# Kernel tuning notes

Measured on AMD Instinct MI355X. Metric: run time of the kernel, lower is better.

The kernel has to match this reference:

```python
import jax, jax.numpy as jnp
import numpy as np

EPS = 1e-5

def _layernorm(x, g, b):
    mu = jnp.mean(x, axis=-1, keepdims=True)
    var = jnp.mean((x - mu) ** 2, axis=-1, keepdims=True)
    return (x - mu) / jnp.sqrt(var + EPS) * g + b


def setup_inputs() -> dict:
    key = jax.random.key(0)
    ks = jax.random.split(key, 4)
    B, H, W, C = 8, 96, 96, 256
    return {
        "x1": jax.random.normal(ks[0], (B, H, W, C), dtype=jnp.float32),
        "x2": jax.random.normal(ks[1], (B, H, W, C), dtype=jnp.float32),
        # norm1 (shared LayerNorm applied to both x1 and x2)
        "g1": jnp.ones((C,), jnp.float32),
        "b1": jnp.zeros((C,), jnp.float32),
        # reprojection 1x1 conv: C -> 2C
        "Wr": jax.random.normal(ks[2], (2 * C, C), dtype=jnp.float32) * 0.05,
        "br": jnp.zeros((2 * C,), jnp.float32),
        # final LayerNorm over 2C
        "g2": jnp.ones((2 * C,), jnp.float32),
        "b2": jnp.zeros((2 * C,), jnp.float32),
        # learnable mixing scalars
        "a1": jnp.array(0.25, jnp.float32),
        "a2": jnp.array(0.25, jnp.float32),
        "a3": jnp.array(0.25, jnp.float32),
        "a4": jnp.array(0.25, jnpp_ := jnp.float32),
    }


def reference(x1, x2, g1, b1, Wr, br, g2, b2, a1, a2, a3, a4):
    B, H, W, C = x1.shape
    N, D = H * W, C  # head_count = 1, key_channels = value_channels = D
    n1 = _layernorm(x1.reshape(B, N, C), g1, b1)  # [B,N,D]
    n2 = _layernorm(x2.reshape(B, N, C), g1, b1)

    kq = jnp.swapaxes(n2, 1, 2)                   # [B,D,N]
    key_sm = jax.nn.softmax(kq, axis=2)           # softmax over N
    query = jax.nn.softmax(kq, axis=1)            # softmax over D
    value = jnp.swapaxes(n1, 1, 2)                # [B,D,N]

    # context = key @ value^T : [B,D,D]
    context = jnp.einsum('bdn,ben->bde', key_sm, value)

    def masked_softmax(k):
        # torch.topk + scatter mask == keep entries >= k-th largest per row
        thr = jax.lax.top_k(context, k)[0][..., -1:]
        return jax.nn.softmax(jnp.where(context >= thr, context, -jnp.inf), axis=-1)

    ks = [D // 2, (D * 2) // 3, (D * 3) // 4, (D * 4) // 5]
    o = [jnp.einsum('bde,ben->bdn', masked_softmax(k), query) for k in ks]
    att = a1 * o[0] + a2 * o[1] + a3 * o[2] + a4 * o[3]  # [B,D,N]

    # 1x1 conv reprojection D -> 2D, then LayerNorm over channels
    rep = jnp.einsum('oc,bcn->bno', Wr, att) + br         # [B,N,2D]
    rep = _layernorm(rep, g2, b2)
    # view(B,H,W,2C).permute(0,3,1,2)
    return jnp.transpose(rep.reshape(B, H, W, 2 * C), (0, 3, 1, 2))
```

## Files before the change

### kernel.cpp

```cpp
#include <hip/hip_runtime.h>
#include <hip/hip_bf16.h>

#define Bc 8
#define Nn 9216
#define Dd 256
#define Oo 512
#define EPSc 1e-5f

#define OFF_MU1    0
#define OFF_RSTD1  73728
#define OFF_MU2    147456
#define OFF_RSTD2  221184
#define OFF_ROWINV 294912
#define OFF_COLSUM 368640
#define OFF_M      894976
#define OFF_W2T    1419264
#define OFF_CTXP   2467840

typedef __attribute__((ext_vector_type(4))) float f32x4;
typedef __attribute__((ext_vector_type(8))) short short8;
typedef __attribute__((ext_vector_type(8))) unsigned short ushort8;

static __device__ __forceinline__ unsigned short f2bf(float f) {
    __hip_bfloat16 h = __float2bfloat16(f);
    union { __hip_bfloat16 hh; unsigned short uu; } cv; cv.hh = h;
    return cv.uu;
}

#define SWZ(ch) (((((ch) >> 2) & 7)) ^ ((((ch) & 3)) << 1))

__global__ __launch_bounds__(256) void mg_k0_zero(float* __restrict__ p, int n4) {
    int i = blockIdx.x * 256 + threadIdx.x;
    if (i < n4) ((float4*)p)[i] = make_float4(0.f, 0.f, 0.f, 0.f);
}

__global__ __launch_bounds__(256) void mg_k1_stats(const float* __restrict__ x1, const float* __restrict__ x2,
                                                   const float* __restrict__ g1, const float* __restrict__ b1,
                                                   float* __restrict__ ws)
{
    float* mu1    = ws + OFF_MU1;
    float* rstd1  = ws + OFF_RSTD1;
    float* mu2    = ws + OFF_MU2;
    float* rstd2  = ws + OFF_RSTD2;
    float* rowinv = ws + OFF_ROWINV;
    float* colsum = ws + OFF_COLSUM;

    int t = threadIdx.x, lane = t & 63, w = t >> 6;
    int b = blockIdx.x / 144, rb = blockIdx.x % 144;
    int nbase = rb * 64;

    float4 g1v = ((const float4*)g1)[lane];
    float4 b1v = ((const float4*)b1)[lane];
    float cs0 = 0.f, cs1 = 0.f, cs2 = 0.f, cs3 = 0.f;
    __shared__ float csL[4][256];

    for (int i = 0; i < 16; ++i) {
        int n = nbase + i * 4 + w;
        int base = (b * Nn + n) * 64 + lane;
        float4 xa = ((const float4*)x1)[base];
        float4 xb = ((const float4*)x2)[base];
        float s1 = xa.x + xa.y + xa.z + xa.w;
        float q1 = xa.x*xa.x + xa.y*xa.y + xa.z*xa.z + xa.w*xa.w;
        float s2 = xb.x + xb.y + xb.z + xb.w;
        float q2 = xb.x*xb.x + xb.y*xb.y + xb.z*xb.z + xb.w*xb.w;
        #pragma unroll
        for (int m = 1; m < 64; m <<= 1) {
            s1 += __shfl_xor(s1, m); q1 += __shfl_xor(q1, m);
            s2 += __shfl_xor(s2, m); q2 += __shfl_xor(q2, m);
        }
        float m1 = s1 * (1.f / Dd), m2 = s2 * (1.f / Dd);
        float r1 = rsqrtf(q1 * (1.f / Dd) - m1 * m1 + EPSc);
        float r2 = rsqrtf(q2 * (1.f / Dd) - m2 * m2 + EPSc);
        int ni = b * Nn + n;
        if (lane == 0) { mu1[ni] = m1; rstd1[ni] = r1; mu2[ni] = m2; rstd2[ni] = r2; }
        float e0 = __expf((xb.x - m2) * r2 * g1v.x + b1v.x);
        float e1 = __expf((xb.y - m2) * r2 * g1v.y + b1v.y);
        float e2 = __expf((xb.z - m2) * r2 * g1v.z + b1v.z);
        float e3 = __expf((xb.w - m2) * r2 * g1v.w + b1v.w);
        float rs = e0 + e1 + e2 + e3;
        #pragma unroll
        for (int m = 1; m < 64; m <<= 1) rs += __shfl_xor(rs, m);
        if (lane == 0) rowinv[ni] = 1.f / rs;
        cs0 += e0; cs1 += e1; cs2 += e2; cs3 += e3;
    }
    csL[w][lane * 4 + 0] = cs0;
    csL[w][lane * 4 + 1] = cs1;
    csL[w][lane * 4 + 2] = cs2;
    csL[w][lane * 4 + 3] = cs3;
    __syncthreads();
    float tot = csL[0][t] + csL[1][t] + csL[2][t] + csL[3][t];
    atomicAdd(&colsum[b * Dd + t], tot);
}

__global__ __launch_bounds__(512, 2) void mg_k3_ctx(const float* __restrict__ x1, const float* __restrict__ x2,
                                                    const float* __restrict__ g1, const float* __restrict__ b1,
                                                    float* __restrict__ ws, int nks)
{
    __shared__ ushort PA[256 * 64];
    __shared__ ushort PB[256 * 64];
    const float* mu1   = ws + OFF_MU1;
    const float* rstd1 = ws + OFF_RSTD1;
    const float* mu2   = ws + OFF_MU2;
    const float* rstd2 = ws + OFF_RSTD2;
    float* ctxp = ws + OFF_CTXP;

    int t = threadIdx.x;
    int ks_i = blockIdx.x % nks;
    int b = blockIdx.x / nks;
    int krange = Nn / nks;
    int ntiles = krange >> 6;
    int n_base = ks_i * krange;

    int o  = t >> 6;
    int c4 = t & 63;

    f32x4 g1v = ((const f32x4*)g1)[c4];
    f32x4 b1v = ((const f32x4*)b1)[c4];

    int lane = t & 63, wave = t >> 6;
    int wd = wave & 3, we = wave >> 2;
    int l15 = lane & 15, kgrp = lane >> 4;

    f32x4 acc[4][8];
    #pragma unroll
    for (int dt = 0; dt < 4; ++dt)
        #pragma unroll
        for (int et = 0; et < 8; ++et) acc[dt][et] = (f32x4){0.f, 0.f, 0.f, 0.f};

    for (int st = 0; st < ntiles; ++st) {
        int rowb = b * Nn + n_base + st * 64 + o * 8;
        __syncthreads();
        {
            f32x4 mv0 = *(const f32x4*)(mu1 + rowb),   mv1 = *(const f32x4*)(mu1 + rowb + 4);
            f32x4 rv0 = *(const f32x4*)(rstd1 + rowb), rv1 = *(const f32x4*)(rstd1 + rowb + 4);
            float mva[8] = {mv0[0], mv0[1], mv0[2], mv0[3], mv1[0], mv1[1], mv1[2], mv1[3]};
            float rva[8] = {rv0[0], rv0[1], rv0[2], rv0[3], rv1[0], rv1[1], rv1[2], rv1[3]};
            f32x4 xv[8];
            #pragma unroll
            for (int rr = 0; rr < 8; ++rr)
                xv[rr] = ((const f32x4*)x1)[(size_t)(rowb + rr) * 64 + c4];
            #pragma unroll
            for (int i = 0; i < 4; ++i) {
                int ch = c4 * 4 + i;
                ushort8 u;
                #pragma unroll
                for (int rr = 0; rr < 8; ++rr)
                    u[rr] = f2bf((xv[rr][i] - mva[rr]) * rva[rr] * g1v[i] + b1v[i]);
                *(ushort8*)&PB[ch * 64 + ((o + SWZ(ch)) & 7) * 8] = u;
            }
        }
        {
            f32x4 mv0 = *(const f32x4*)(mu2 + rowb),   mv1 = *(const f32x4*)(mu2 + rowb + 4);
            f32x4 rv0 = *(const f32x4*)(rstd2 + rowb), rv1 = *(const f32x4*)(rstd2 + rowb + 4);
            float mva[8] = {mv0[0], mv0[1], mv0[2], mv0[3], mv1[0], mv1[1], mv1[2], mv1[3]};
            float rva[8] = {rv0[0], rv0[1], rv0[2], rv0[3], rv1[0], rv1[1], rv1[2], rv1[3]};
            f32x4 xv[8];
            #pragma unroll
            for (int rr = 0; rr < 8; ++rr)
                xv[rr] = ((const f32x4*)x2)[(size_t)(rowb + rr) * 64 + c4];
            #pragma unroll
            for (int i = 0; i < 4; ++i) {
                int ch = c4 * 4 + i;
                ushort8 u;
                #pragma unroll
                for (int rr = 0; rr < 8; ++rr)
                    u[rr] = f2bf(__expf((xv[rr][i] - mva[rr]) * rva[rr] * g1v[i] + b1v[i]));
                *(ushort8*)&PA[ch * 64 + ((o + SWZ(ch)) & 7) * 8] = u;
            }
        }
        __syncthreads();

        #pragma unroll
        for (int kk = 0; kk < 2; ++kk) {
            short8 af[4], bf[8];
            #pragma unroll
            for (int dt = 0; dt < 4; ++dt) {
                int ch = wd * 64 + dt * 16 + l15;
                af[dt] = *(const short8*)&PA[ch * 64 + (((kk << 2) + kgrp + SWZ(ch)) & 7) * 8];
            }
            #pragma unroll
            for (int et = 0; et < 8; ++et) {
                int ch = we * 128 + et * 16 + l15;
                bf[et] = *(const short8*)&PB[ch * 64 + (((kk << 2) + kgrp + SWZ(ch)) & 7) * 8];
            }
            #pragma unroll
            for (int dt = 0; dt < 4; ++dt)
                #pragma unroll
                for (int et = 0; et < 8; ++et)
                    acc[dt][et] = __builtin_amdgcn_mfma_f32_16x16x32_bf16(af[dt], bf[et], acc[dt][et], 0, 0, 0);
        }
    }

    size_t obase = ((size_t)ks_i * Bc + b) * (Dd * Dd);
    #pragma unroll
    for (int dt = 0; dt < 4; ++dt) {
        #pragma unroll
        for (int r = 0; r < 4; ++r) {
            int d = wd * 64 + dt * 16 + kgrp * 4 + r;
            float* rowp = ctxp + obase + (size_t)d * Dd + we * 128 + l15;
            #pragma unroll
            for (int et = 0; et < 8; ++et)
                rowp[et * 16] = acc[dt][et][r];
        }
    }
}

__global__ __launch_bounds__(256) void mg_k5_mask(const float* __restrict__ a1p, const float* __restrict__ a2p,
                                                  const float* __restrict__ a3p, const float* __restrict__ a4p,
                                                  float* __restrict__ ws, int nks)
{
    const float* ctxp   = ws + OFF_CTXP;
    const float* colsum = ws + OFF_COLSUM;
    float* Mo = ws + OFF_M;
    int t = threadIdx.x;
    int b = blockIdx.x >> 8, d = blockIdx.x & 255;
    __shared__ float s[256];
    __shared__ float wred[4][4];

    float c = 0.f;
    for (int p = 0; p < nks; ++p)
        c += ctxp[((size_t)p * Bc + b) * (Dd * Dd) + (size_t)d * Dd + t];
    float inv = 1.f / colsum[b * Dd + d];
    c *= inv;
    s[t] = c;
    __syncthreads();
    for (int k = 2; k <= 256; k <<= 1) {
        for (int j = k >> 1; j > 0; j >>= 1) {
            int ixj = t ^ j;
            if (ixj > t) {
                float A = s[t], Bv = s[ixj];
                bool desc = ((t & k) == 0);
                bool sw = desc ? (A < Bv) : (A > Bv);
                if (sw) { s[t] = Bv; s[ixj] = A; }
            }
            __syncthreads();
        }
    }
    float cmax = s[0];
    float t0 = s[127], t1 = s[169], t2 = s[191], t3 = s[203];
    float e = __expf(c - cmax);
    float w0 = (c >= t0) ? e : 0.f;
    float w1 = (c >= t1) ? e : 0.f;
    float w2 = (c >= t2) ? e : 0.f;
    float w3 = (c >= t3) ? e : 0.f;
    float v0 = w0, v1 = w1, v2 = w2, v3 = w3;
    #pragma unroll
    for (int m = 1; m < 64; m <<= 1) {
        v0 += __shfl_xor(v0, m); v1 += __shfl_xor(v1, m);
        v2 += __shfl_xor(v2, m); v3 += __shfl_xor(v3, m);
    }
    int lane = t & 63, wv = t >> 6;
    if (lane == 0) { wred[wv][0] = v0; wred[wv][1] = v1; wred[wv][2] = v2; wred[wv][3] = v3; }
    __syncthreads();
    float S0 = wred[0][0] + wred[1][0] + wred[2][0] + wred[3][0];
    float S1 = wred[0][1] + wred[1][1] + wred[2][1] + wred[3][1];
    float S2 = wred[0][2] + wred[1][2] + wred[2][2] + wred[3][2];
    float S3 = wred[0][3] + wred[1][3] + wred[2][3] + wred[3][3];
    float Mv = a1p[0] * (w0 / S0) + a2p[0] * (w1 / S1) + a3p[0] * (w2 / S2) + a4p[0] * (w3 / S3);
    Mo[(b * Dd + d) * Dd + t] = Mv;
}

__global__ __launch_bounds__(256) void mg_k6_w2(const float* __restrict__ Wr, float* __restrict__ ws)
{
    const float* Mo = ws + OFF_M;
    ushort* W2B = (ushort*)(ws + OFF_W2T);
    __shared__ float Mt[32][128];
    __shared__ float WrT[32][36];
    int t = threadIdx.x;
    int b = blockIdx.x >> 5, ob = (blockIdx.x >> 1) & 15, eh = blockIdx.x & 1;
    int o0 = ob * 32, e0 = eh * 128;
    int ol4 = t & 7, el = t >> 3;
    float acc[4][4];
    #pragma unroll
    for (int i = 0; i < 4; ++i)
        #pragma unroll
        for (int j = 0; j < 4; ++j) acc[i][j] = 0.f;

    for (int ch = 0; ch < 8; ++ch) {
        int c0 = ch * 32;
        __syncthreads();
        #pragma unroll
        for (int k = 0; k < 4; ++k) {
            int fi = t + k * 256;
            int row = fi >> 5, c4 = fi & 31;
            float4 mv = ((const float4*)Mo)[(b * Dd + c0 + row) * 64 + (e0 >> 2) + c4];
            *(float4*)&Mt[row][c4 * 4] = mv;
        }
        {
            int ol = t >> 3, c4 = t & 7;
            float4 wv = ((const float4*)Wr)[(o0 + ol) * 64 + (c0 >> 2) + c4];
            WrT[c4 * 4 + 0][ol] = wv.x;
            WrT[c4 * 4 + 1][ol] = wv.y;
            WrT[c4 * 4 + 2][ol] = wv.z;
            WrT[c4 * 4 + 3][ol] = wv.w;
        }
        __syncthreads();
        #pragma unroll
        for (int cc = 0; cc < 32; ++cc) {
            float4 w4 = *(const float4*)&WrT[cc][ol4 * 4];
            float4 m4 = *(const float4*)&Mt[cc][el * 4];
            float wv[4] = {w4.x, w4.y, w4.z, w4.w};
            float mv[4] = {m4.x, m4.y, m4.z, m4.w};
            #pragma unroll
            for (int i = 0; i < 4; ++i)
                #pragma unroll
                for (int j = 0; j < 4; ++j)
                    acc[i][j] = fmaf(wv[i], mv[j], acc[i][j]);
        }
    }
    #pragma unroll
    for (int i = 0; i < 4; ++i) {
        int o = o0 + ol4 * 4 + i;
        ushort4 u;
        u.x = f2bf(acc[i][0]); u.y = f2bf(acc[i][1]);
        u.z = f2bf(acc[i][2]); u.w = f2bf(acc[i][3]);
        *(ushort4*)&W2B[((size_t)b * Oo + o) * Dd + e0 + el * 4] = u;
    }
}

__global__ __launch_bounds__(256, 2) void mg_k7_final(const float* __restrict__ x2,
        const float* __restrict__ g1, const float* __restrict__ b1,
        const float* __restrict__ br, const float* __restrict__ g2, const float* __restrict__ b2,
        const float* __restrict__ ws, float* __restrict__ out)
{
    __shared__ ushort qsT[64 * 256];
    __shared__ float stat[4][4][16][2];
    __shared__ float musig[64][2];

    const float* mu2    = ws + OFF_MU2;
    const float* rstd2  = ws + OFF_RSTD2;
    const float* rowinv = ws + OFF_ROWINV;
    const ushort* W2B   = (const ushort*)(ws + OFF_W2T);

    int t = threadIdx.x;
    int b = blockIdx.x / 144, nt0 = blockIdx.x % 144;
    int n0 = nt0 * 64;

    {
        int row = t >> 2, gb = (t & 3) * 8;
        int ni = b * Nn + n0 + row;
        float m = mu2[ni], r = rstd2[ni], ri = rowinv[ni];
        #pragma unroll
        for (int j = 0; j < 8; ++j) {
            int g = gb + j;
            int e = g * 8;
            const float4* xp = (const float4*)x2 + (size_t)ni * 64 + g * 2;
            float4 xa = xp[0], xb = xp[1];
            float4 ga = ((const float4*)g1)[g * 2], gb4 = ((const float4*)g1)[g * 2 + 1];
            float4 ba = ((const float4*)b1)[g * 2], bb4 = ((const float4*)b1)[g * 2 + 1];
            float v[8]  = {xa.x, xa.y, xa.z, xa.w, xb.x, xb.y, xb.z, xb.w};
            float gv[8] = {ga.x, ga.y, ga.z, ga.w, gb4.x, gb4.y, gb4.z, gb4.w};
            float bv[8] = {ba.x, ba.y, ba.z, ba.w, bb4.x, bb4.y, bb4.z, bb4.w};
            ushort8 u;
            #pragma unroll
            for (int q = 0; q < 8; ++q)
                u[q] = f2bf(__expf((v[q] - m) * r * gv[q] + bv[q]) * ri);
            (void)e;
            *(ushort8*)&qsT[row * 256 + ((g ^ (row & 7)) << 3)] = u;
        }
    }
    __syncthreads();

    int lw = t & 63, wave = t >> 6;
    int colA = lw & 15, kgrp = lw >> 4;

    f32x4 acc[8][4];
    #pragma unroll
    for (int ot = 0; ot < 8; ++ot)
        #pragma unroll
        for (int nt = 0; nt < 4; ++nt)
            acc[ot][nt] = (f32x4){0.f, 0.f, 0.f, 0.f};

    const ushort* abase = W2B + ((size_t)b * Oo + wave * 128 + colA) * Dd + kgrp * 8;

#define LOADAF(dst, ksv)                                                        \
    {                                                                           \
        _Pragma("unroll")                                                       \
        for (int ot = 0; ot < 8; ++ot)                                          \
            dst[ot] = *(const short8*)&abase[(size_t)ot * 16 * Dd + (ksv) * 32];\
    }

#define MFMASTEP(afv, ksv)                                                      \
    {                                                                           \
        short8 bf[4];                                                           \
        int gsl = (((ksv) * 4 + kgrp) ^ (colA & 7)) << 3;                       \
        _Pragma("unroll")                                                       \
        for (int nt = 0; nt < 4; ++nt)                                          \
            bf[nt] = *(const short8*)&qsT[(nt * 16 + colA) * 256 + gsl];        \
        _Pragma("unroll")                                                       \
        for (int ot = 0; ot < 8; ++ot)                                          \
            _Pragma("unroll")                                                   \
            for (int nt = 0; nt < 4; ++nt)                                      \
                acc[ot][nt] = __builtin_amdgcn_mfma_f32_16x16x32_bf16(          \
                    afv[ot], bf[nt], acc[ot][nt], 0, 0, 0);                     \
    }

    short8 afA[8], afB[8];
    LOADAF(afA, 0);
    #pragma unroll
    for (int kp = 0; kp < 4; ++kp) {
        LOADAF(afB, 2 * kp + 1);
        MFMASTEP(afA, 2 * kp);
        if (kp < 3) LOADAF(afA, 2 * kp + 2);
        MFMASTEP(afB, 2 * kp + 1);
    }
#undef LOADAF
#undef MFMASTEP

    float ps[4] = {0.f, 0.f, 0.f, 0.f}, pq[4] = {0.f, 0.f, 0.f, 0.f};
    #pragma unroll
    for (int ot = 0; ot < 8; ++ot) {
        #pragma unroll
        for (int r = 0; r < 4; ++r) {
            int o = wave * 128 + ot * 16 + kgrp * 4 + r;
            float bb = br[o];
            #pragma unroll
            for (int nt = 0; nt < 4; ++nt) {
                float v = acc[ot][nt][r] + bb;
                acc[ot][nt][r] = v;
                ps[nt] += v; pq[nt] += v * v;
            }
        }
    }
    #pragma unroll
    for (int m = 16; m <= 32; m <<= 1) {
        #pragma unroll
        for (int nt = 0; nt < 4; ++nt) {
            ps[nt] += __shfl_xor(ps[nt], m);
            pq[nt] += __shfl_xor(pq[nt], m);
        }
    }
    if (lw < 16) {
        #pragma unroll
        for (int nt = 0; nt < 4; ++nt) {
            stat[wave][nt][lw][0] = ps[nt];
            stat[wave][nt][lw][1] = pq[nt];
        }
    }
    __syncthreads();
    if (t < 64) {
        int ntl = t >> 4, col = t & 15;
        float S = 0.f, Q = 0.f;
        #pragma unroll
        for (int w2 = 0; w2 < 4; ++w2) { S += stat[w2][ntl][col][0]; Q += stat[w2][ntl][col][1]; }
        float mu = S * (1.f / Oo);
        float var = Q * (1.f / Oo) - mu * mu;
        musig[t][0] = mu;
        musig[t][1] = rsqrtf(var + EPSc);
    }
    __syncthreads();

    float mn[4], rs[4];
    #pragma unroll
    for (int nt = 0; nt < 4; ++nt) {
        mn[nt] = musig[nt * 16 + colA][0];
        rs[nt] = musig[nt * 16 + colA][1];
    }
    #pragma unroll
    for (int ot = 0; ot < 8; ++ot) {
        #pragma unroll
        for (int r = 0; r < 4; ++r) {
            int o = wave * 128 + ot * 16 + kgrp * 4 + r;
            float gg = g2[o], bb2 = b2[o];
            size_t ob = ((size_t)b * Oo + o) * Nn + n0;
            #pragma unroll
            for (int nt = 0; nt < 4; ++nt)
                out[ob + nt * 16 + colA] = (acc[ot][nt][r] - mn[nt]) * rs[nt] * gg + bb2;
        }
    }
}

extern "C" void kernel_launch(void* const* d_in, const int* in_sizes, int n_in,
                              void* d_out, int out_size, void* d_ws, size_t ws_size,
                              hipStream_t stream)
{
    (void)in_sizes; (void)n_in; (void)out_size;
    const float* x1 = (const float*)d_in[0];
    const float* x2 = (const float*)d_in[1];
    const float* g1 = (const float*)d_in[2];
    const float* b1 = (const float*)d_in[3];
    const float* Wr = (const float*)d_in[4];
    const float* br = (const float*)d_in[5];
    const float* g2 = (const float*)d_in[6];
    const float* b2 = (const float*)d_in[7];
    const float* a1 = (const float*)d_in[8];
    const float* a2 = (const float*)d_in[9];
    const float* a3 = (const float*)d_in[10];
    const float* a4 = (const float*)d_in[11];
    float* ws = (float*)d_ws;
    float* out = (float*)d_out;

    const int cand[6] = {24, 16, 12, 8, 4, 2};
    int nks = 2;
    for (int ci = 0; ci < 6; ++ci) {
        if ((2467840ull + (size_t)cand[ci] * 524288ull) * 4ull <= ws_size) { nks = cand[ci]; break; }
    }

    hipLaunchKernelGGL(mg_k0_zero, dim3(2), dim3(256), 0, stream, ws + OFF_COLSUM, 512);
    hipLaunchKernelGGL(mg_k1_stats, dim3(1152), dim3(256), 0, stream, x1, x2, g1, b1, ws);
    hipLaunchKernelGGL(mg_k3_ctx, dim3(Bc * nks), dim3(512), 0, stream, x1, x2, g1, b1, ws, nks);
    hipLaunchKernelGGL(mg_k5_mask, dim3(2048), dim3(256), 0, stream, a1, a2, a3, a4, ws, nks);
    hipLaunchKernelGGL(mg_k6_w2, dim3(256), dim3(256), 0, stream, Wr, ws);
    hipLaunchKernelGGL(mg_k7_final, dim3(1152), dim3(256), 0, stream, x2, g1, b1, br, g2, b2, ws, out);
}
```

Before: 216.8 us.

## Precompute bf16 query softmax in stats kernel and widen final GEMM blocks

The stats kernel now writes the channel-softmax query directly as bf16 into a new workspace buffer. The final kernel then loads it instead of re-reading fp32 x2 and recomputing exp and the normalisation, which halves the bytes read for that operand and removes the duplicate transcendental work. W2 is stored in a k-slice-blocked layout, and the final kernel uses 512 threads with 8 waves, each covering 64 output channels, which lowers per-thread accumulator pressure. The cost is an extra bf16 write of the whole query tensor (about 38MB), a larger workspace offset, and a rowinv buffer that is no longer used. The candidate split count for the context kernel also gains a larger option.

```diff
diff --git a/kernel.cpp b/kernel.cpp
--- a/kernel.cpp
+++ b/kernel.cpp
@@ -11,11 +11,11 @@
 #define OFF_RSTD1  73728
 #define OFF_MU2    147456
 #define OFF_RSTD2  221184
-#define OFF_ROWINV 294912
-#define OFF_COLSUM 368640
-#define OFF_M      894976
-#define OFF_W2T    1419264
-#define OFF_CTXP   2467840
+#define OFF_COLSUM 294912
+#define OFF_M      296960
+#define OFF_W2T    821248
+#define OFF_QB     1345536
+#define OFF_CTXP   10782720
 
 typedef __attribute__((ext_vector_type(4))) float f32x4;
 typedef __attribute__((ext_vector_type(8))) short short8;
@@ -42,8 +42,8 @@
     float* rstd1  = ws + OFF_RSTD1;
     float* mu2    = ws + OFF_MU2;
     float* rstd2  = ws + OFF_RSTD2;
-    float* rowinv = ws + OFF_ROWINV;
     float* colsum = ws + OFF_COLSUM;
+    ushort* qb    = (ushort*)(ws + OFF_QB);
 
     int t = threadIdx.x, lane = t & 63, w = t >> 6;
     int b = blockIdx.x / 144, rb = blockIdx.x % 144;
@@ -80,7 +80,11 @@
         float rs = e0 + e1 + e2 + e3;
         #pragma unroll
         for (int m = 1; m < 64; m <<= 1) rs += __shfl_xor(rs, m);
-        if (lane == 0) rowinv[ni] = 1.f / rs;
+        float ri = 1.f / rs;
+        ushort4 uq;
+        uq.x = f2bf(e0 * ri); uq.y = f2bf(e1 * ri);
+        uq.z = f2bf(e2 * ri); uq.w = f2bf(e3 * ri);
+        *(ushort4*)&qb[(size_t)ni * 256 + lane * 4] = uq;
         cs0 += e0; cs1 += e1; cs2 += e2; cs3 += e3;
     }
     csL[w][lane * 4 + 0] = cs0;
@@ -308,54 +312,42 @@
                     acc[i][j] = fmaf(wv[i], mv[j], acc[i][j]);
         }
     }
-    #pragma unroll
-    for (int i = 0; i < 4; ++i) {
-        int o = o0 + ol4 * 4 + i;
-        ushort4 u;
-        u.x = f2bf(acc[i][0]); u.y = f2bf(acc[i][1]);
-        u.z = f2bf(acc[i][2]); u.w = f2bf(acc[i][3]);
-        *(ushort4*)&W2B[((size_t)b * Oo + o) * Dd + e0 + el * 4] = u;
-    }
-}
-
-__global__ __launch_bounds__(256, 2) void mg_k7_final(const float* __restrict__ x2,
-        const float* __restrict__ g1, const float* __restrict__ b1,
+    {
+        int ee = e0 + el * 4;
+        int ks = ee >> 5, eloc = ee & 31;
+        #pragma unroll
+        for (int i = 0; i < 4; ++i) {
+            int o = o0 + ol4 * 4 + i;
+            ushort4 u;
+            u.x = f2bf(acc[i][0]); u.y = f2bf(acc[i][1]);
+            u.z = f2bf(acc[i][2]); u.w = f2bf(acc[i][3]);
+            *(ushort4*)&W2B[(((size_t)b * 8 + ks) * Oo + o) * 32 + eloc] = u;
+        }
+    }
+}
+
+__global__ __launch_bounds__(512, 4) void mg_k7_final(
         const float* __restrict__ br, const float* __restrict__ g2, const float* __restrict__ b2,
         const float* __restrict__ ws, float* __restrict__ out)
 {
     __shared__ ushort qsT[64 * 256];
-    __shared__ float stat[4][4][16][2];
+    __shared__ float stat[8][4][16][2];
     __shared__ float musig[64][2];
 
-    const float* mu2    = ws + OFF_MU2;
-    const float* rstd2  = ws + OFF_RSTD2;
-    const float* rowinv = ws + OFF_ROWINV;
-    const ushort* W2B   = (const ushort*)(ws + OFF_W2T);
+    const ushort* qb  = (const ushort*)(ws + OFF_QB);
+    const ushort* W2B = (const ushort*)(ws + OFF_W2T);
 
     int t = threadIdx.x;
     int b = blockIdx.x / 144, nt0 = blockIdx.x % 144;
     int n0 = nt0 * 64;
 
     {
-        int row = t >> 2, gb = (t & 3) * 8;
-        int ni = b * Nn + n0 + row;
-        float m = mu2[ni], r = rstd2[ni], ri = rowinv[ni];
-        #pragma unroll
-        for (int j = 0; j < 8; ++j) {
-            int g = gb + j;
-            int e = g * 8;
-            const float4* xp = (const float4*)x2 + (size_t)ni * 64 + g * 2;
-            float4 xa = xp[0], xb = xp[1];
-            float4 ga = ((const float4*)g1)[g * 2], gb4 = ((const float4*)g1)[g * 2 + 1];
-            float4 ba = ((const float4*)b1)[g * 2], bb4 = ((const float4*)b1)[g * 2 + 1];
-            float v[8]  = {xa.x, xa.y, xa.z, xa.w, xb.x, xb.y, xb.z, xb.w};
-            float gv[8] = {ga.x, ga.y, ga.z, ga.w, gb4.x, gb4.y, gb4.z, gb4.w};
-            float bv[8] = {ba.x, ba.y, ba.z, ba.w, bb4.x, bb4.y, bb4.z, bb4.w};
-            ushort8 u;
-            #pragma unroll
-            for (int q = 0; q < 8; ++q)
-                u[q] = f2bf(__expf((v[q] - m) * r * gv[q] + bv[q]) * ri);
-            (void)e;
+        int row = t >> 3, gq = (t & 7) * 4;
+        size_t ni = (size_t)(b * Nn + n0 + row);
+        #pragma unroll
+        for (int jj = 0; jj < 4; ++jj) {
+            int g = gq + jj;
+            ushort8 u = *(const ushort8*)&qb[ni * 256 + g * 8];
             *(ushort8*)&qsT[row * 256 + ((g ^ (row & 7)) << 3)] = u;
         }
     }
@@ -364,38 +356,38 @@
     int lw = t & 63, wave = t >> 6;
     int colA = lw & 15, kgrp = lw >> 4;
 
-    f32x4 acc[8][4];
-    #pragma unroll
-    for (int ot = 0; ot < 8; ++ot)
+    f32x4 acc[4][4];
+    #pragma unroll
+    for (int ot = 0; ot < 4; ++ot)
         #pragma unroll
         for (int nt = 0; nt < 4; ++nt)
             acc[ot][nt] = (f32x4){0.f, 0.f, 0.f, 0.f};
 
-    const ushort* abase = W2B + ((size_t)b * Oo + wave * 128 + colA) * Dd + kgrp * 8;
-
-#define LOADAF(dst, ksv)                                                        \
-    {                                                                           \
-        _Pragma("unroll")                                                       \
-        for (int ot = 0; ot < 8; ++ot)                                          \
-            dst[ot] = *(const short8*)&abase[(size_t)ot * 16 * Dd + (ksv) * 32];\
-    }
-
-#define MFMASTEP(afv, ksv)                                                      \
-    {                                                                           \
-        short8 bf[4];                                                           \
-        int gsl = (((ksv) * 4 + kgrp) ^ (colA & 7)) << 3;                       \
-        _Pragma("unroll")                                                       \
-        for (int nt = 0; nt < 4; ++nt)                                          \
-            bf[nt] = *(const short8*)&qsT[(nt * 16 + colA) * 256 + gsl];        \
-        _Pragma("unroll")                                                       \
-        for (int ot = 0; ot < 8; ++ot)                                          \
-            _Pragma("unroll")                                                   \
-            for (int nt = 0; nt < 4; ++nt)                                      \
-                acc[ot][nt] = __builtin_amdgcn_mfma_f32_16x16x32_bf16(          \
-                    afv[ot], bf[nt], acc[ot][nt], 0, 0, 0);                     \
-    }
-
-    short8 afA[8], afB[8];
+    const ushort* abase = W2B + ((size_t)b * 8 * Oo + wave * 64 + colA) * 32 + kgrp * 8;
+
+#define LOADAF(dst, ksv)                                                         \
+    {                                                                            \
+        _Pragma("unroll")                                                        \
+        for (int ot = 0; ot < 4; ++ot)                                           \
+            dst[ot] = *(const short8*)&abase[((size_t)(ksv) * Oo + ot * 16) * 32];\
+    }
+
+#define MFMASTEP(afv, ksv)                                                       \
+    {                                                                            \
+        int gsl = (((ksv) * 4 + kgrp) ^ (colA & 7)) << 3;                        \
+        short8 bf[4];                                                            \
+        _Pragma("unroll")                                                        \
+        for (int nt = 0; nt < 4; ++nt)                                           \
+            bf[nt] = *(const short8*)&qsT[(nt * 16 + colA) * 256 + gsl];         \
+        _Pragma("unroll")                                                        \
+        for (int ot = 0; ot < 4; ++ot)                                           \
+            _Pragma("unroll")                                                    \
+            for (int nt = 0; nt < 4; ++nt)                                       \
+                acc[ot][nt] = __builtin_amdgcn_mfma_f32_16x16x32_bf16(           \
+                    afv[ot], bf[nt], acc[ot][nt], 0, 0, 0);                      \
+    }
+
+    short8 afA[4], afB[4];
     LOADAF(afA, 0);
     #pragma unroll
     for (int kp = 0; kp < 4; ++kp) {
@@ -409,10 +401,10 @@
 
     float ps[4] = {0.f, 0.f, 0.f, 0.f}, pq[4] = {0.f, 0.f, 0.f, 0.f};
     #pragma unroll
-    for (int ot = 0; ot < 8; ++ot) {
+    for (int ot = 0; ot < 4; ++ot) {
         #pragma unroll
         for (int r = 0; r < 4; ++r) {
-            int o = wave * 128 + ot * 16 + kgrp * 4 + r;
+            int o = wave * 64 + ot * 16 + kgrp * 4 + r;
             float bb = br[o];
             #pragma unroll
             for (int nt = 0; nt < 4; ++nt) {
@@ -442,7 +434,7 @@
         int ntl = t >> 4, col = t & 15;
         float S = 0.f, Q = 0.f;
         #pragma unroll
-        for (int w2 = 0; w2 < 4; ++w2) { S += stat[w2][ntl][col][0]; Q += stat[w2][ntl][col][1]; }
+        for (int w2 = 0; w2 < 8; ++w2) { S += stat[w2][ntl][col][0]; Q += stat[w2][ntl][col][1]; }
         float mu = S * (1.f / Oo);
         float var = Q * (1.f / Oo) - mu * mu;
         musig[t][0] = mu;
@@ -457,10 +449,10 @@
         rs[nt] = musig[nt * 16 + colA][1];
     }
     #pragma unroll
-    for (int ot = 0; ot < 8; ++ot) {
+    for (int ot = 0; ot < 4; ++ot) {
         #pragma unroll
         for (int r = 0; r < 4; ++r) {
-            int o = wave * 128 + ot * 16 + kgrp * 4 + r;
+            int o = wave * 64 + ot * 16 + kgrp * 4 + r;
             float gg = g2[o], bb2 = b2[o];
             size_t ob = ((size_t)b * Oo + o) * Nn + n0;
             #pragma unroll
@@ -490,10 +482,10 @@
     float* ws = (float*)d_ws;
     float* out = (float*)d_out;
 
-    const int cand[6] = {24, 16, 12, 8, 4, 2};
+    const int cand[7] = {36, 24, 16, 12, 8, 4, 2};
     int nks = 2;
-    for (int ci = 0; ci < 6; ++ci) {
-        if ((2467840ull + (size_t)cand[ci] * 524288ull) * 4ull <= ws_size) { nks = cand[ci]; break; }
+    for (int ci = 0; ci < 7; ++ci) {
+        if (((size_t)OFF_CTXP + (size_t)cand[ci] * 524288ull) * 4ull <= ws_size) { nks = cand[ci]; break; }
     }
 
     hipLaunchKernelGGL(mg_k0_zero, dim3(2), dim3(256), 0, stream, ws + OFF_COLSUM, 512);
@@ -501,5 +493,5 @@
     hipLaunchKernelGGL(mg_k3_ctx, dim3(Bc * nks), dim3(512), 0, stream, x1, x2, g1, b1, ws, nks);
     hipLaunchKernelGGL(mg_k5_mask, dim3(2048), dim3(256), 0, stream, a1, a2, a3, a4, ws, nks);
     hipLaunchKernelGGL(mg_k6_w2, dim3(256), dim3(256), 0, stream, Wr, ws);
-    hipLaunchKernelGGL(mg_k7_final, dim3(1152), dim3(256), 0, stream, x2, g1, b1, br, g2, b2, ws, out);
-}
+    hipLaunchKernelGGL(mg_k7_final, dim3(1152), dim3(512), 0, stream, br, g2, b2, ws, out);
+}
```

Result: no change. 220.8 us (+1.9%).
